# Kernel optimization log

Hardware: AMD Instinct MI355X
Metric: run time of the kernel (lower is better)

## Reference

```python
import jax, jax.numpy as jnp
import numpy as np
import math

B, CIN, COUT, NSC, H, W = 4, 3, 64, 3, 192, 192
HID = 64  # attention hidden channels


def setup_inputs() -> dict:
    key = jax.random.key(0)
    ks = jax.random.split(key, 10)
    pi = math.pi
    return {
        "x": jax.random.normal(ks[0], (B, CIN, H, W), jnp.float32),
        "freq": jax.random.uniform(ks[1], (NSC, COUT, CIN), jnp.float32) * pi,
        "theta": jax.random.uniform(ks[2], (NSC, COUT, CIN), jnp.float32) * pi,
        "sigma": jax.random.uniform(ks[3], (NSC, COUT, CIN), jnp.float32) * pi,
        "f0": jnp.ones((NSC, COUT, CIN), jnp.float32),
        "theta0": jnp.ones((NSC, COUT, CIN), jnp.float32),
        "attn_w1": jax.random.normal(ks[4], (HID, CIN), jnp.float32) / np.sqrt(CIN).astype(np.float32),
        "attn_b1": jnp.zeros((HID,), jnp.float32),
        "attn_w2": jax.random.normal(ks[5], (COUT * NSC, HID), jnp.float32) / np.sqrt(HID).astype(np.float32),
        "attn_b2": jnp.zeros((COUT * NSC,), jnp.float32),
        "bn_w": jnp.ones((COUT * NSC,), jnp.float32),
        "bn_b": jnp.zeros((COUT * NSC,), jnp.float32),
        "mixing_param": jax.random.uniform(ks[6], (1,), jnp.float32),
        "conv_w": jax.random.normal(ks[7], (COUT, CIN, 3, 3), jnp.float32) * 0.1,
        "freq_band_select": jax.random.uniform(ks[8], (COUT, CIN, 2), jnp.float32),
    }


def _forward(x, freq, theta, sigma, f0, theta0, attn_w1, attn_b1, attn_w2,
             attn_b2, bn_w, bn_b, mixing_param, conv_w, freq_band_select):
    b, cin, h, w = x.shape
    # torch.fft.fftshift default dim=None shifts ALL axes (incl. batch/channel)
    Xs = jnp.fft.fftshift(jnp.fft.fft2(x))  # [B,Cin,H,W] complex64

    # ---- multi-scale log-Gabor filter bank g[S,O,I,H,W] ----
    yy, xx = jnp.meshgrid(jnp.linspace(-1.0, 1.0, h), jnp.linspace(-1.0, 1.0, w), indexing="ij")
    r = jnp.sqrt(xx * xx + yy * yy + 1e-6)
    phi = jnp.arctan2(yy, xx)
    f0e = f0[..., None, None]
    sg = sigma[..., None, None]
    th = theta[..., None, None]
    th0 = theta0[..., None, None]
    fr = freq[..., None, None]
    log_gabor = jnp.exp(-(jnp.log(r) - jnp.log(f0e)) ** 2 / (2.0 * jnp.log(sg / f0e) ** 2))
    angular = jnp.exp(-(phi - th) ** 2 / (2.0 * th0 ** 2))
    g = log_gabor * angular * jnp.cos(fr * r) / (2.0 * math.pi * sg ** 2)  # [S,O,I,H,W]

    # ---- frequency attention: 1x1 conv -> ReLU -> 1x1 conv -> BN(train) -> softmax ----
    mag = jnp.abs(Xs)
    h1 = jax.nn.relu(jnp.einsum("oi,bihw->bohw", attn_w1, mag) + attn_b1[None, :, None, None])
    h2 = jnp.einsum("oi,bihw->bohw", attn_w2, h1) + attn_b2[None, :, None, None]
    mu = h2.mean(axis=(0, 2, 3))
    var = h2.var(axis=(0, 2, 3))  # biased, as torch BN training mode
    h2 = (h2 - mu[None, :, None, None]) * jax.lax.rsqrt(var + 1e-5)[None, :, None, None]
    h2 = h2 * bn_w[None, :, None, None] + bn_b[None, :, None, None]
    attn = jax.nn.softmax(h2, axis=1).reshape(b, NSC, COUT, h, w)  # view as [B,S,O,H,W]

    # ---- attention-weighted complex sum over (scale, out, in), then batch ----
    # attended_output(b) = sum_{s,o,i} attn[b,s,o]*g[s,o,i]*Xs[b,i]; torch then
    # sums over Cin and, via the [B,O,B,I,H,W] broadcast + sum(dims 2,3), over batch.
    Wr = jnp.einsum("bsohw,soihw->bihw", attn, g)  # real attention*filter weights
    A_tot = (Wr * Xs).sum(axis=(0, 1))             # [H,W] complex

    # ---- per-(out,in) frequency band mask (same index range on both axes) ----
    idx = jnp.floor((freq_band_select + 1.0) * 0.5 * h).astype(jnp.int32)  # [O,I,2]
    hr = jnp.arange(h)
    c = (hr[None, None, :] >= idx[..., 0:1]) & (hr[None, None, :] < idx[..., 1:2])  # [O,I,H]
    mask = (c[:, :, :, None] & c[:, :, None, :]).astype(jnp.float32)  # [O,I,H,W]
    Msum = mask.sum(axis=1)  # [O,H,W] (sum over Cin)

    # torch builds r[b0,o,b2,i,h,w]=A[b2]*M[o,i], ifftshift(all axes), ifft2,
    # real, sum over (b2,i). Rolls on summed axes commute with the sums, so this
    # equals ifftshift over (b0,o,h,w) of Q[b0,o]=A_tot*Msum[o] (const in b0).
    Q = jnp.broadcast_to((A_tot[None] * Msum.astype(Xs.dtype))[None], (b, COUT, h, w))
    xf = jnp.fft.ifft2(jnp.fft.ifftshift(Q)).real  # [B,O,H,W]

    xs = jax.lax.conv_general_dilated(
        x, conv_w, window_strides=(1, 1), padding=((1, 1), (1, 1)),
        dimension_numbers=("NCHW", "OIHW", "NCHW"))
    return mixing_param * xf + (1.0 - mixing_param) * xs


def reference(x, freq, theta, sigma, f0, theta0, attn_w1, attn_b1, attn_w2,
              attn_b2, bn_w, bn_b, mixing_param, conv_w, freq_band_select):
    return _forward(x, freq, theta, sigma, f0, theta0, attn_w1, attn_b1,
                    attn_w2, attn_b2, bn_w, bn_b, mixing_param, conv_w,
                    freq_band_select)
```

## Files before the change

### kernel.cpp

```cpp
#include <hip/hip_runtime.h>
#include <math.h>

#define NPIX  36864
#define PI2   6.28318530717958647692f

#define TW_OFF    0
#define PCA_OFF   1536
#define PCB_OFF   10752
#define W1F4_OFF  15360
#define W2B_OFF   16384
#define BN_OFF    65536
#define IDX_OFF   67072
#define M2_OFF    68608
#define T1_OFF    85248
#define XS_OFF    3624192
#define AH_OFF    7163136
#define XF_OFF    7458048
#define E2B_OFF   15846656
#define WS_FUSED  7458048
#define WS_SPLIT  16895232

#define PH_BYTES  14155776
#define E2C_OFF   14155776
#define OUT_MIN_ELEMS 9437184

typedef __attribute__((ext_vector_type(8))) short short8;
typedef __attribute__((ext_vector_type(4))) float floatx4;

__device__ __forceinline__ void bf16split(float v, unsigned short& hi, unsigned short& lo) {
    unsigned ub = __builtin_bit_cast(unsigned, v);
    hi = (unsigned short)(ub >> 16);
    float vh = __builtin_bit_cast(float, ub & 0xFFFF0000u);
    lo = (unsigned short)(__builtin_bit_cast(unsigned, v - vh) >> 16);
}

__global__ void k_pre(const float* freq, const float* theta, const float* sigma,
                      const float* f0, const float* theta0, const float* fbs,
                      const float* w1, const float* b1v, const float* w2,
                      char* ws, char* outw, int split) {
    float2* tw   = (float2*)(ws + TW_OFF);
    float4* pcA  = (float4*)(ws + PCA_OFF);
    float2* pcB  = (float2*)(ws + PCB_OFF);
    float4* w1f4 = (float4*)(ws + W1F4_OFF);
    unsigned short* w2b = (unsigned short*)(ws + W2B_OFF);
    int* idx = (int*)(ws + IDX_OFF);
    int gtid = blockIdx.x * blockDim.x + threadIdx.x;
    int gsz  = gridDim.x * blockDim.x;
    for (int n = gtid; n < 192; n += gsz) {
        float th = PI2 * (float)n / 192.0f;
        tw[n] = make_float2(cosf(th), sinf(th));
    }
    for (int t = gtid; t < 576; t += gsz) {
        int s = t / 192, rem = t % 192, o = rem / 3, i = rem % 3;
        float fr = freq[t], th = theta[t], sg = sigma[t], f0v = f0[t], th0 = theta0[t];
        float lg  = logf(sg / f0v);
        float a1  = -1.0f / (2.0f * lg * lg);
        float lf0 = logf(f0v);
        float a2  = -1.0f / (2.0f * th0 * th0);
        float lsc = -logf(PI2 * sg * sg);
        int pidx = (s*3 + i)*64 + o;
        pcA[pidx] = make_float4(a1, lf0, a2, th);
        pcB[pidx] = make_float2(fr, lsc);
    }
    for (int t = gtid; t < 64; t += gsz)
        w1f4[t] = make_float4(w1[t*3+0], w1[t*3+1], w1[t*3+2], b1v[t]);
    for (int u = gtid; u < 24576; u += gsz) {
        int j = u & 7; int v = u >> 3;
        int l = v & 63; v >>= 6;
        int hsel = v & 1; v >>= 1;
        int t = v % 12; int kc = v / 12;
        int k = kc*32 + (l>>4)*8 + j;
        int c = t*16 + (l & 15);
        float wv = w2[c*64 + k];
        unsigned short hi, lo;
        bf16split(wv, hi, lo);
        w2b[u] = hsel ? lo : hi;
    }
    for (int t = gtid; t < 192; t += gsz) {
        int lo = (int)floorf((fbs[t*2+0] + 1.0f) * 0.5f * 192.0f) - 96;
        int hi = (int)floorf((fbs[t*2+1] + 1.0f) * 0.5f * 192.0f) - 96;
        lo = max(0, min(96, lo));
        hi = max(0, min(96, hi));
        if (hi < lo) hi = lo;
        idx[t*2+0] = lo; idx[t*2+1] = hi;
    }
    if (split) {
        unsigned short* e2b = (unsigned short*)(ws + E2B_OFF);
        for (int u = gtid; u < 147456; u += gsz) {
            int j = u & 7;
            int l = (u >> 3) & 63;
            int half = (u >> 9) & 1;
            int rest = u >> 10;
            int kc = rest % 12, t = rest / 12;
            int k = kc*32 + ((l >> 4) << 3) + j;
            int w = k >> 1, comp = k & 1;
            int n = t*16 + (l & 15);
            int ang = (w * n) % 192;
            float th = PI2 * (float)ang / 192.0f;
            float v = comp ? sinf(th) : cosf(th);
            unsigned short hi, lo;
            bf16split(v, hi, lo);
            e2b[u] = half ? lo : hi;
        }
        unsigned short* e2c = (unsigned short*)(outw + E2C_OFF);
        for (int u = gtid; u < 73728; u += gsz) {
            int j = u & 7;
            int l = (u >> 3) & 63;
            int half = (u >> 9) & 1;
            int rest = u >> 10;
            int kc = rest % 6, t = rest / 6;
            int k = kc*32 + ((l >> 4) << 3) + j;
            int w = k >> 1, comp = k & 1;
            int n = t*16 + (l & 15);
            int ang = (w * n) % 192;
            float th = PI2 * (float)ang / 192.0f;
            float v = comp ? sinf(th) : cosf(th);
            unsigned short hi, lo;
            bf16split(v, hi, lo);
            e2c[u] = half ? lo : hi;
        }
    }
}

__global__ __launch_bounds__(192) void k_dft1s(const float* x, char* ws) {
    __shared__ float2 twsh[192];
    const float2* tw = (const float2*)(ws + TW_OFF);
    int tid = threadIdx.x;
    twsh[tid] = tw[tid];
    __syncthreads();
    int bi = blockIdx.x;
    int y0 = blockIdx.y * 4;
    int z  = blockIdx.z;
    float2* t1 = (float2*)(ws + (z ? XF_OFF : T1_OFF));
    int w  = tid;
    const float* xp = x + bi * NPIX;
    float2 acc[4];
#pragma unroll
    for (int d = 0; d < 4; d++) acc[d] = make_float2(0.f, 0.f);
    int h0 = z * 96;
    for (int h = h0; h < h0 + 96; h++) {
        float xv = xp[h*192 + w];
        int m = (h * y0) % 192;
#pragma unroll
        for (int d = 0; d < 4; d++) {
            float2 e = twsh[m];
            acc[d].x += xv * e.x;
            acc[d].y -= xv * e.y;
            m += h; if (m >= 192) m -= 192;
        }
    }
    float2* op = t1 + bi * NPIX;
#pragma unroll
    for (int d = 0; d < 4; d++) op[(y0 + d)*192 + w] = acc[d];
}

__global__ __launch_bounds__(192) void k_dft1(const float* x, char* ws) {
    __shared__ float2 twsh[192];
    const float2* tw = (const float2*)(ws + TW_OFF);
    float2* t1 = (float2*)(ws + T1_OFF);
    int tid = threadIdx.x;
    twsh[tid] = tw[tid];
    __syncthreads();
    int bi = blockIdx.x;
    int y0 = blockIdx.y * 4;
    int w  = tid;
    const float* xp = x + bi * NPIX;
    float2 acc[4];
#pragma unroll
    for (int d = 0; d < 4; d++) acc[d] = make_float2(0.f, 0.f);
    for (int h = 0; h < 192; h++) {
        float xv = xp[h*192 + w];
        int m = (h * y0) % 192;
#pragma unroll
        for (int d = 0; d < 4; d++) {
            float2 e = twsh[m];
            acc[d].x += xv * e.x;
            acc[d].y -= xv * e.y;
            m += h; if (m >= 192) m -= 192;
        }
    }
    float2* op = t1 + bi * NPIX;
#pragma unroll
    for (int d = 0; d < 4; d++) op[(y0 + d)*192 + w] = acc[d];
}

__global__ __launch_bounds__(256) void k_dft2m(char* ws) {
    __shared__ __align__(16) float2 Ar[16][194];
    const float2* t1a = (const float2*)(ws + T1_OFF);
    const float2* t1b = (const float2*)(ws + XF_OFF);
    const unsigned short* e2b = (const unsigned short*)(ws + E2B_OFF);
    float2* Xs = (float2*)(ws + XS_OFF);
    int tid = threadIdx.x;
    int bi = blockIdx.x / 12;
    int y0 = (blockIdx.x % 12) * 16;
    for (int u = tid; u < 3072; u += 256) {
        int m = u / 192, w = u - m*192;
        float2 v = t1a[bi*NPIX + (y0+m)*192 + w];
        float2 v2 = t1b[bi*NPIX + (y0+m)*192 + w];
        v.x += v2.x; v.y += v2.y;
        Ar[m][w] = v;
    }
    __syncthreads();
    int wave = tid >> 6, lane = tid & 63;
    int ml = lane & 15, qd = lane >> 4;
    floatx4 accre[3], accim[3];
#pragma unroll
    for (int tt = 0; tt < 3; tt++) {
        accre[tt] = (floatx4){0.f,0.f,0.f,0.f};
        accim[tt] = (floatx4){0.f,0.f,0.f,0.f};
    }
    union AB { short8 v; unsigned short u[8]; };
#pragma unroll 1
    for (int kc = 0; kc < 12; kc++) {
        int wb = kc*16 + qd*4;
        float4 p01 = *(const float4*)&Ar[ml][wb];
        float4 p23 = *(const float4*)&Ar[ml][wb + 2];
        float av[8]  = {p01.x, p01.y, p01.z, p01.w, p23.x, p23.y, p23.z, p23.w};
        float apv[8] = {p01.y, -p01.x, p01.w, -p01.z, p23.y, -p23.x, p23.w, -p23.z};
        AB ah, al, aph, apl;
#pragma unroll
        for (int j = 0; j < 8; j++) {
            bf16split(av[j],  ah.u[j],  al.u[j]);
            bf16split(apv[j], aph.u[j], apl.u[j]);
        }
#pragma unroll
        for (int tt = 0; tt < 3; tt++) {
            int t = wave*3 + tt;
            const unsigned short* bp = e2b + (((t*12 + kc)*2) << 9) + (lane << 3);
            short8 bh = *(const short8*)bp;
            short8 bl = *(const short8*)(bp + 512);
            floatx4 r = accre[tt];
            r = __builtin_amdgcn_mfma_f32_16x16x32_bf16(ah.v,  bh, r, 0, 0, 0);
            r = __builtin_amdgcn_mfma_f32_16x16x32_bf16(al.v,  bh, r, 0, 0, 0);
            r = __builtin_amdgcn_mfma_f32_16x16x32_bf16(ah.v,  bl, r, 0, 0, 0);
            accre[tt] = r;
            floatx4 q = accim[tt];
            q = __builtin_amdgcn_mfma_f32_16x16x32_bf16(aph.v, bh, q, 0, 0, 0);
            q = __builtin_amdgcn_mfma_f32_16x16x32_bf16(apl.v, bh, q, 0, 0, 0);
            q = __builtin_amdgcn_mfma_f32_16x16x32_bf16(aph.v, bl, q, 0, 0, 0);
            accim[tt] = q;
        }
    }
    int b = bi / 3, i = bi % 3;
    int bs = (b + 2) & 3;
    int is = (i + 1) % 3;
    float2* Xp = Xs + (bs*3 + is)*NPIX;
#pragma unroll
    for (int tt = 0; tt < 3; tt++) {
        int kx = (wave*3 + tt)*16 + ml;
        int ks = kx + 96; if (ks >= 192) ks -= 192;
#pragma unroll
        for (int r = 0; r < 4; r++) {
            int y = y0 + qd*4 + r;
            int ys = y + 96; if (ys >= 192) ys -= 192;
            Xp[ys*192 + ks] = make_float2(accre[tt][r], accim[tt][r]);
        }
    }
}

__global__ __launch_bounds__(192) void k_dft2(char* ws, int split) {
    __shared__ float2 twsh[192];
    __shared__ float2 row[192];
    const float2* tw = (const float2*)(ws + TW_OFF);
    const float2* t1a = (const float2*)(ws + T1_OFF);
    const float2* t1b = (const float2*)(ws + XF_OFF);
    float2* Xs = (float2*)(ws + XS_OFF);
    int tid = threadIdx.x;
    int bi = blockIdx.x, y = blockIdx.y;
    twsh[tid] = tw[tid];
    {
        float2 v = t1a[bi*NPIX + y*192 + tid];
        if (split) {
            float2 v2 = t1b[bi*NPIX + y*192 + tid];
            v.x += v2.x; v.y += v2.y;
        }
        row[tid] = v;
    }
    __syncthreads();
    int kx = tid;
    float2 st = twsh[kx];
    float2 acc = make_float2(0.f, 0.f);
#pragma unroll 1
    for (int w0 = 0; w0 < 192; w0 += 32) {
        float2 e = twsh[(w0 * kx) % 192];
#pragma unroll
        for (int w = 0; w < 32; w++) {
            float2 t = row[w0 + w];
            acc.x += t.x*e.x + t.y*e.y;
            acc.y += t.y*e.x - t.x*e.y;
            float ex = e.x*st.x - e.y*st.y;
            e.y = e.x*st.y + e.y*st.x;
            e.x = ex;
        }
    }
    int b = bi / 3, i = bi % 3;
    int bs = (b + 2) & 3;
    int is = (i + 1) % 3;
    int ys = y + 96;  if (ys >= 192) ys -= 192;
    int ks = kx + 96; if (ks >= 192) ks -= 192;
    Xs[(bs*3 + is)*NPIX + ys*192 + ks] = acc;
}

__global__ __launch_bounds__(256) void k_stats(char* ws) {
    __shared__ float magL[192];
    __shared__ float4 w1L[64];
    __shared__ float m1L[64];
    __shared__ __align__(16) unsigned short fragH[512*8];
    __shared__ __align__(16) unsigned short fragL[512*8];
    const float2* Xs = (const float2*)(ws + XS_OFF);
    float* M2 = (float*)(ws + M2_OFF);
    int tid = threadIdx.x;
    int wave = tid >> 6, lane = tid & 63;
    if (tid < 64) { w1L[tid] = ((const float4*)(ws + W1F4_OFF))[tid]; m1L[tid] = 0.f; }
    __syncthreads();
    int cch = wave*16 + (lane & 15);
    float4 wf = w1L[cch];
    float msum = 0.f;
    floatx4 acc[4];
#pragma unroll
    for (int nb = 0; nb < 4; nb++) acc[nb] = (floatx4){0.f, 0.f, 0.f, 0.f};
    union AB { short8 v; unsigned short u[8]; };
#pragma unroll 1
    for (int it = 0; it < 2; it++) {
        int tile = blockIdx.x * 2 + it;
        int S0 = tile * 64;
        int b = S0 / NPIX;
        int p0 = S0 - b*NPIX;
        if (tid < 192) {
            int i = tid >> 6, s = tid & 63;
            float2 v = Xs[(b*3 + i)*NPIX + p0 + s];
            magL[s*3 + i] = sqrtf(v.x*v.x + v.y*v.y);
        }
        __syncthreads();
#pragma unroll
        for (int kc = 0; kc < 2; kc++) {
            AB h8, l8;
#pragma unroll
            for (int j = 0; j < 8; j++) {
                int s = kc*32 + (lane>>4)*8 + j;
                float mg0 = magL[s*3], mg1 = magL[s*3+1], mg2 = magL[s*3+2];
                float hv = fmaxf(wf.w + wf.x*mg0 + wf.y*mg1 + wf.z*mg2, 0.f);
                msum += hv;
                bf16split(hv, h8.u[j], l8.u[j]);
            }
            int z = (kc*4 + wave)*64 + lane;
            *(short8*)&fragH[z*8] = h8.v;
            *(short8*)&fragL[z*8] = l8.v;
        }
        __syncthreads();
        short8 Ah0 = *(const short8*)&fragH[((0*4+wave)*64 + lane)*8];
        short8 Ah1 = *(const short8*)&fragH[((1*4+wave)*64 + lane)*8];
        short8 Al0 = *(const short8*)&fragL[((0*4+wave)*64 + lane)*8];
        short8 Al1 = *(const short8*)&fragL[((1*4+wave)*64 + lane)*8];
#pragma unroll
        for (int nb = 0; nb < 4; nb++) {
            short8 Bh0 = *(const short8*)&fragH[((0*4+nb)*64 + lane)*8];
            short8 Bh1 = *(const short8*)&fragH[((1*4+nb)*64 + lane)*8];
            short8 Bl0 = *(const short8*)&fragL[((0*4+nb)*64 + lane)*8];
            short8 Bl1 = *(const short8*)&fragL[((1*4+nb)*64 + lane)*8];
            floatx4 a = acc[nb];
            a = __builtin_amdgcn_mfma_f32_16x16x32_bf16(Ah0, Bh0, a, 0, 0, 0);
            a = __builtin_amdgcn_mfma_f32_16x16x32_bf16(Al0, Bh0, a, 0, 0, 0);
            a = __builtin_amdgcn_mfma_f32_16x16x32_bf16(Ah0, Bl0, a, 0, 0, 0);
            a = __builtin_amdgcn_mfma_f32_16x16x32_bf16(Ah1, Bh1, a, 0, 0, 0);
            a = __builtin_amdgcn_mfma_f32_16x16x32_bf16(Al1, Bh1, a, 0, 0, 0);
            a = __builtin_amdgcn_mfma_f32_16x16x32_bf16(Ah1, Bl1, a, 0, 0, 0);
            acc[nb] = a;
        }
        __syncthreads();
    }
#pragma unroll
    for (int nb = 0; nb < 4; nb++)
#pragma unroll
        for (int r = 0; r < 4; r++) {
            int row = wave*16 + (lane>>4)*4 + r;
            int col = nb*16 + (lane & 15);
            atomicAdd(&M2[row*64 + col], acc[nb][r]);
        }
    atomicAdd(&m1L[cch], msum);
    __syncthreads();
    if (tid < 64) atomicAdd(&M2[4096 + tid], m1L[tid]);
}

__global__ __launch_bounds__(64) void k_bn(const float* w2, const float* bnw,
                                           const float* bnb, char* ws) {
    const float* M2 = (const float*)(ws + M2_OFF);
    const float* m1 = M2 + 4096;
    float* bnsc = (float*)(ws + BN_OFF);
    float* bnsh = bnsc + 192;
    int c = blockIdx.x;
    int jj = threadIdx.x;
    const float* row = w2 + c*64;
    float rj = row[jj];
    float inner = 0.f;
    const float* m2r = M2 + jj*64;
    for (int k = 0; k < 64; k++) inner += row[k] * m2r[k];
    float qpart = rj * inner;
    float dpart = rj * m1[jj];
#pragma unroll
    for (int sh = 32; sh >= 1; sh >>= 1) {
        qpart += __shfl_xor(qpart, sh);
        dpart += __shfl_xor(dpart, sh);
    }
    if (jj == 0) {
        const float invN = 1.0f / 147456.0f;
        float d = dpart * invN;
        float qv = qpart * invN;
        float var = qv - d*d;
        float rstd = rsqrtf(var + 1e-5f);
        float scale = bnw[c] * rstd;
        bnsc[c] = scale;
        bnsh[c] = bnb[c] - d * scale;
    }
}

__global__ __launch_bounds__(256) void k_attn(char* ws) {
    __shared__ __align__(16) float4 pcAL[576];
    __shared__ float2 pcBL[576];
    __shared__ float4 w1L[64];
    const float2* Xs = (const float2*)(ws + XS_OFF);
    const float* bnA = (const float*)(ws + BN_OFF);
    const char* W2G = (const char*)(ws + W2B_OFF);
    float2* Ah = (float2*)(ws + AH_OFF);
    int tid = threadIdx.x;
    {
        const float4* pcA4 = (const float4*)(ws + PCA_OFF);
        const float2* pcB2 = (const float2*)(ws + PCB_OFF);
        for (int u = tid; u < 576; u += 256) {
            pcAL[u] = pcA4[u];
            pcBL[u] = pcB2[u];
        }
        if (tid < 64) w1L[tid] = ((const float4*)(ws + W1F4_OFF))[tid];
    }
    __syncthreads();
    int wave = tid >> 6, lane = tid & 63;
    int cl = lane & 15, q = lane >> 4;
    int g = blockIdx.x * 4 + wave;
    int pix0 = g * 4;

    union AB { short8 v; unsigned short u[8]; };
    int pb = pix0 + (cl >> 2), bb = cl & 3;
    float2 q0 = Xs[(bb*3+0)*NPIX + pb];
    float2 q1 = Xs[(bb*3+1)*NPIX + pb];
    float2 q2 = Xs[(bb*3+2)*NPIX + pb];
    float mg0 = sqrtf(q0.x*q0.x + q0.y*q0.y);
    float mg1 = sqrtf(q1.x*q1.x + q1.y*q1.y);
    float mg2 = sqrtf(q2.x*q2.x + q2.y*q2.y);
    AB ah[2], al[2];
#pragma unroll
    for (int kc = 0; kc < 2; kc++)
#pragma unroll
        for (int j = 0; j < 8; j++) {
            int k = kc*32 + q*8 + j;
            float4 wf = w1L[k];
            float hv = fmaxf(wf.w + wf.x*mg0 + wf.y*mg1 + wf.z*mg2, 0.f);
            bf16split(hv, ah[kc].u[j], al[kc].u[j]);
        }
    int pixE = pix0 + q;
    int hh = pixE / 192, ww = pixE - hh*192;
    float yy = -1.0f + (float)hh * (2.0f/191.0f);
    float xx = -1.0f + (float)ww * (2.0f/191.0f);
    float rr = sqrtf(xx*xx + yy*yy + 1e-6f);
    float lr = __logf(rr);
    float phi = atan2f(yy, xx);
    float sm0 = 0.f, sm1 = 0.f, sm2 = 0.f, sm3 = 0.f;
    float Wr[4][3];
#pragma unroll
    for (int r = 0; r < 4; r++) { Wr[r][0] = 0.f; Wr[r][1] = 0.f; Wr[r][2] = 0.f; }
#pragma unroll 2
    for (int t = 0; t < 12; t++) {
        floatx4 a = {0.f, 0.f, 0.f, 0.f};
#pragma unroll
        for (int kc = 0; kc < 2; kc++) {
            int ob = (((kc*12 + t)*2)*64 + lane)*16;
            short8 bh = *(const short8*)(W2G + ob);
            short8 bl = *(const short8*)(W2G + ob + 1024);
            a = __builtin_amdgcn_mfma_f32_16x16x32_bf16(ah[kc].v, bh, a, 0, 0, 0);
            a = __builtin_amdgcn_mfma_f32_16x16x32_bf16(al[kc].v, bh, a, 0, 0, 0);
            a = __builtin_amdgcn_mfma_f32_16x16x32_bf16(ah[kc].v, bl, a, 0, 0, 0);
        }
        int c = t*16 + cl;
        float sc_ = bnA[c], sh_ = bnA[192 + c];
        float e0 = __expf(a[0]*sc_ + sh_);
        float e1 = __expf(a[1]*sc_ + sh_);
        float e2 = __expf(a[2]*sc_ + sh_);
        float e3 = __expf(a[3]*sc_ + sh_);
        sm0 += e0; sm1 += e1; sm2 += e2; sm3 += e3;
        int sB = c >> 6, o = c & 63;
#pragma unroll
        for (int i = 0; i < 3; i++) {
            int pidx = (sB*3 + i)*64 + o;
            float4 pa = pcAL[pidx];
            float2 pbv = pcBL[pidx];
            float dl = lr - pa.y, dp = phi - pa.w;
            float gv = __expf(pa.x*dl*dl + pa.z*dp*dp + pbv.y) * __cosf(pbv.x*rr);
            Wr[0][i] += e0*gv; Wr[1][i] += e1*gv;
            Wr[2][i] += e2*gv; Wr[3][i] += e3*gv;
        }
    }
#pragma unroll
    for (int sh = 1; sh < 16; sh <<= 1) {
        sm0 += __shfl_xor(sm0, sh); sm1 += __shfl_xor(sm1, sh);
        sm2 += __shfl_xor(sm2, sh); sm3 += __shfl_xor(sm3, sh);
    }
    float inv0 = 1.0f/sm0, inv1 = 1.0f/sm1, inv2 = 1.0f/sm2, inv3 = 1.0f/sm3;
    float are = 0.f, aim = 0.f;
#pragma unroll
    for (int i = 0; i < 3; i++) {
        float2 x0 = Xs[(0*3+i)*NPIX + pixE];
        float2 x1 = Xs[(1*3+i)*NPIX + pixE];
        float2 x2 = Xs[(2*3+i)*NPIX + pixE];
        float2 x3 = Xs[(3*3+i)*NPIX + pixE];
        float w0v = Wr[0][i]*inv0, w1v = Wr[1][i]*inv1;
        float w2v = Wr[2][i]*inv2, w3v = Wr[3][i]*inv3;
        are += w0v*x0.x + w1v*x1.x + w2v*x2.x + w3v*x3.x;
        aim += w0v*x0.y + w1v*x1.y + w2v*x2.y + w3v*x3.y;
    }
#pragma unroll
    for (int sh = 1; sh < 16; sh <<= 1) {
        are += __shfl_xor(are, sh);
        aim += __shfl_xor(aim, sh);
    }
    if (cl == 0) {
        int hs = hh + 96; if (hs >= 192) hs -= 192;
        int wsx = ww + 96; if (wsx >= 192) wsx -= 192;
        Ah[hs*192 + wsx] = make_float2(are, aim);
    }
}

__global__ __launch_bounds__(192) void k_phpre(char* ws, char* outw) {
    __shared__ float2 AhL[96];
    const float2* tw  = (const float2*)(ws + TW_OFF);
    const float2* Ahp = (const float2*)(ws + AH_OFF);
    float2* Ph = (float2*)outw;
    int y = threadIdx.x;
    int w = blockIdx.x;
    if (y < 96) AhL[y] = Ahp[y*192 + w];
    __syncthreads();
    float2 step = tw[y];
    float ex = 1.f, ey = 0.f;
    float ax = 0.f, ay = 0.f;
    for (int h = 0; h < 96; h++) {
        float2 a = AhL[h];
        ax += a.x*ex - a.y*ey;
        ay += a.x*ey + a.y*ex;
        Ph[(h*96 + w)*192 + y] = make_float2(ax, ay);
        float t = ex*step.x - ey*step.y;
        ey = ex*step.y + ey*step.x;
        ex = t;
    }
}

__global__ __launch_bounds__(256) void k_ifftm(char* ws, char* outw) {
    __shared__ __align__(16) unsigned short AhiL[16*200];
    __shared__ __align__(16) unsigned short AloL[16*200];
    __shared__ int iL[3], iH[3];
    const float2* Ph = (const float2*)outw;
    const unsigned short* e2c = (const unsigned short*)(outw + E2C_OFF);
    const int* idx = (const int*)(ws + IDX_OFF);
    float* xf = (float*)(ws + XF_OFF);
    int tid = threadIdx.x;
    int o  = blockIdx.x / 12;
    int ys = blockIdx.x % 12;
    int op = (o + 32) & 63;
    if (tid < 3) { iL[tid] = idx[(op*3 + tid)*2]; iH[tid] = idx[(op*3 + tid)*2 + 1]; }
    __syncthreads();
    for (int u = tid; u < 1536; u += 256) {
        int w = u >> 4, yy = u & 15;
        int y = ys*16 + yy;
        float sr = 0.f, si = 0.f;
#pragma unroll
        for (int i = 0; i < 3; i++) {
            int lo = iL[i], hi = iH[i];
            if (w >= lo && w < hi) {
                float2 a = Ph[((hi-1)*96 + w)*192 + y];
                sr += a.x; si += a.y;
                if (lo > 0) {
                    float2 b2 = Ph[((lo-1)*96 + w)*192 + y];
                    sr -= b2.x; si -= b2.y;
                }
            }
        }
        unsigned short rh, rl, ih, il;
        bf16split(sr, rh, rl);
        bf16split(-si, ih, il);
        *(unsigned*)&AhiL[yy*200 + 2*w] = (unsigned)rh | ((unsigned)ih << 16);
        *(unsigned*)&AloL[yy*200 + 2*w] = (unsigned)rl | ((unsigned)il << 16);
    }
    __syncthreads();
    int wave = tid >> 6, lane = tid & 63;
    int ml = lane & 15, qd = lane >> 4;
    const float s = 1.0f / 36864.0f;
#pragma unroll 1
    for (int ntl = 0; ntl < 3; ntl++) {
        int nt = wave*3 + ntl;
        floatx4 acc = (floatx4){0.f,0.f,0.f,0.f};
#pragma unroll
        for (int kc = 0; kc < 6; kc++) {
            const unsigned short* bp = e2c + ((nt*6 + kc) << 10) + (lane << 3);
            short8 bh = *(const short8*)bp;
            short8 bl = *(const short8*)(bp + 512);
            int ka = kc*32 + qd*8;
            short8 ah = *(const short8*)&AhiL[ml*200 + ka];
            short8 al = *(const short8*)&AloL[ml*200 + ka];
            acc = __builtin_amdgcn_mfma_f32_16x16x32_bf16(ah, bh, acc, 0, 0, 0);
            acc = __builtin_amdgcn_mfma_f32_16x16x32_bf16(al, bh, acc, 0, 0, 0);
            acc = __builtin_amdgcn_mfma_f32_16x16x32_bf16(ah, bl, acc, 0, 0, 0);
        }
#pragma unroll
        for (int r = 0; r < 4; r++) {
            int y = ys*16 + qd*4 + r;
            int x = nt*16 + ml;
            xf[o*NPIX + y*192 + x] = acc[r] * s;
        }
    }
}

__global__ __launch_bounds__(192) void k_conv(const float* x, const float* convw,
                                              const float* mixp, const float* xf,
                                              float* out) {
    int col = threadIdx.x;
    int y = blockIdx.x;
    int b = blockIdx.y;
    float xv[27];
#pragma unroll
    for (int i = 0; i < 3; i++)
#pragma unroll
        for (int dy = 0; dy < 3; dy++)
#pragma unroll
            for (int dx = 0; dx < 3; dx++) {
                int yq = y + dy - 1, xq = col + dx - 1;
                bool ok = (yq >= 0) & (yq < 192) & (xq >= 0) & (xq < 192);
                xv[(i*3 + dy)*3 + dx] = ok ? x[(b*3+i)*NPIX + yq*192 + xq] : 0.f;
            }
    float mixv = mixp[0];
    float onem = 1.0f - mixv;
    for (int o = 0; o < 64; o++) {
        float s = 0.f;
#pragma unroll
        for (int c = 0; c < 27; c++) s += xv[c] * convw[o*27 + c];
        float xfv = xf[o*NPIX + y*192 + col];
        out[((b*64 + o)*192 + y)*192 + col] = mixv*xfv + onem*s;
    }
}

__global__ __launch_bounds__(192) void k_final(const float* x, const float* convw,
                                               const float* mixp, float* out, char* ws) {
    __shared__ float2 twsh[192];
    __shared__ float2 Ssh[3][96];
    __shared__ float cwsh[27];
    __shared__ int iL[3], iH[3];
    const float2* tw = (const float2*)(ws + TW_OFF);
    const int* idx = (const int*)(ws + IDX_OFF);
    const float2* Ah = (const float2*)(ws + AH_OFF);
    int tid = threadIdx.x;
    int y = blockIdx.x;
    int o = blockIdx.y;
    int op = (o + 32) & 63;
    twsh[tid] = tw[tid];
    if (tid < 27) cwsh[tid] = convw[o*27 + tid];
    if (tid < 3) { iL[tid] = idx[(op*3 + tid)*2]; iH[tid] = idx[(op*3 + tid)*2 + 1]; }
    __syncthreads();
    int l0 = iL[0], u0 = iH[0], l1 = iL[1], u1 = iH[1], l2 = iL[2], u2 = iH[2];
    int n0 = u0 - l0, n1 = u1 - l1, n2 = u2 - l2;
    int p1 = n0 + n1, T = p1 + n2;
    for (int t = tid; t < T; t += 192) {
        int i, off, lo, hi;
        if (t < n0)      { i = 0; off = t;      lo = l0; hi = u0; }
        else if (t < p1) { i = 1; off = t - n0; lo = l1; hi = u1; }
        else             { i = 2; off = t - p1; lo = l2; hi = u2; }
        int wq = lo + off;
        float sx = 0.f, sy = 0.f;
        int m = (lo * y) % 192;
        for (int hq = lo; hq < hi; hq++) {
            float2 a = Ah[hq*192 + wq];
            float2 e = twsh[m];
            sx += a.x*e.x - a.y*e.y;
            sy += a.x*e.y + a.y*e.x;
            m += y; if (m >= 192) m -= 192;
        }
        Ssh[i][off] = make_float2(sx, sy);
    }
    __syncthreads();
    int col = tid;
    float accre = 0.f;
#pragma unroll
    for (int i = 0; i < 3; i++) {
        int lo = iL[i];
        int wi = iH[i] - lo;
        int m = (lo * col) % 192;
        for (int off = 0; off < wi; off++) {
            float2 S = Ssh[i][off];
            float2 e = twsh[m];
            accre += S.x*e.x - S.y*e.y;
            m += col; if (m >= 192) m -= 192;
        }
    }
    float xfv = accre * (1.0f / 36864.0f);
    float mixv = mixp[0];
    float onem = 1.0f - mixv;
#pragma unroll
    for (int b = 0; b < 4; b++) {
        float s = 0.f;
#pragma unroll
        for (int i = 0; i < 3; i++) {
            const float* xp = x + (b*3 + i)*NPIX;
#pragma unroll
            for (int dy = -1; dy <= 1; dy++) {
                int yq = y + dy;
                if (yq < 0 || yq >= 192) continue;
                const float* rowp = xp + yq*192;
#pragma unroll
                for (int dx = -1; dx <= 1; dx++) {
                    int xq = col + dx;
                    if (xq < 0 || xq >= 192) continue;
                    s += rowp[xq] * cwsh[i*9 + (dy+1)*3 + (dx+1)];
                }
            }
        }
        out[((b*64 + o)*192 + y)*192 + col] = mixv*xfv + onem*s;
    }
}

extern "C" void kernel_launch(void* const* d_in, const int* in_sizes, int n_in,
                              void* d_out, int out_size, void* d_ws, size_t ws_size,
                              hipStream_t stream) {
    const float* x      = (const float*)d_in[0];
    const float* freq   = (const float*)d_in[1];
    const float* theta  = (const float*)d_in[2];
    const float* sigma  = (const float*)d_in[3];
    const float* f0     = (const float*)d_in[4];
    const float* theta0 = (const float*)d_in[5];
    const float* aw1    = (const float*)d_in[6];
    const float* ab1    = (const float*)d_in[7];
    const float* aw2    = (const float*)d_in[8];
    const float* bnw    = (const float*)d_in[10];
    const float* bnb    = (const float*)d_in[11];
    const float* mixp   = (const float*)d_in[12];
    const float* convw  = (const float*)d_in[13];
    const float* fbs    = (const float*)d_in[14];
    float* out = (float*)d_out;
    char* ws = (char*)d_ws;
    char* outc = (char*)d_out;
    if (ws_size < (size_t)WS_FUSED) return;
    int split = (ws_size >= (size_t)WS_SPLIT) && (out_size >= OUT_MIN_ELEMS);

    hipMemsetAsync(ws + M2_OFF, 0, 16640, stream);
    k_pre  <<<80, 256, 0, stream>>>(freq, theta, sigma, f0, theta0, fbs,
                                    aw1, ab1, aw2, ws, outc, split);
    if (split) {
        k_dft1s<<<dim3(12, 48, 2), 192, 0, stream>>>(x, ws);
        k_dft2m<<<144, 256, 0, stream>>>(ws);
    } else {
        k_dft1 <<<dim3(12, 48), 192, 0, stream>>>(x, ws);
        k_dft2 <<<dim3(12, 192), 192, 0, stream>>>(ws, 0);
    }
    k_stats<<<1152, 256, 0, stream>>>(ws);
    k_bn   <<<192, 64, 0, stream>>>(aw2, bnw, bnb, ws);
    k_attn <<<2304, 256, 0, stream>>>(ws);
    if (split) {
        k_phpre<<<96, 192, 0, stream>>>(ws, outc);
        k_ifftm<<<768, 256, 0, stream>>>(ws, outc);
        k_conv <<<dim3(192, 4), 192, 0, stream>>>(x, convw, mixp,
                                                  (const float*)(ws + XF_OFF), out);
    } else {
        k_final<<<dim3(192, 64), 192, 0, stream>>>(x, convw, mixp, out, ws);
    }
}
```

Measured before the change: 271.7 us.

## Fuse row DFT into column MFMA kernel using bf16-split twiddle matrices

```diff
diff --git a/kernel.cpp b/kernel.cpp
--- a/kernel.cpp
+++ b/kernel.cpp
@@ -102,6 +102,24 @@
             bf16split(v, hi, lo);
             e2b[u] = half ? lo : hi;
         }
+        unsigned short* e1 = (unsigned short*)(ws + T1_OFF);
+        for (int u = gtid; u < 147456; u += gsz) {
+            int j = u & 7;
+            int l = (u >> 3) & 63;
+            int half = (u >> 9) & 1;
+            int rest = u >> 10;
+            int kc = rest % 6;
+            int comp = (rest / 6) & 1;
+            int yt = rest / 12;
+            int y = yt*16 + (l & 15);
+            int h = kc*32 + ((l >> 4) << 3) + j;
+            int ang = (h * y) % 192;
+            float th = PI2 * (float)ang / 192.0f;
+            float v = comp ? -sinf(th) : cosf(th);
+            unsigned short hi, lo;
+            bf16split(v, hi, lo);
+            e1[u] = half ? lo : hi;
+        }
         unsigned short* e2c = (unsigned short*)(outw + E2C_OFF);
         for (int u = gtid; u < 73728; u += gsz) {
             int j = u & 7;
@@ -122,94 +140,69 @@
     }
 }
 
-__global__ __launch_bounds__(192) void k_dft1s(const float* x, char* ws) {
-    __shared__ float2 twsh[192];
-    const float2* tw = (const float2*)(ws + TW_OFF);
-    int tid = threadIdx.x;
-    twsh[tid] = tw[tid];
-    __syncthreads();
-    int bi = blockIdx.x;
-    int y0 = blockIdx.y * 4;
-    int z  = blockIdx.z;
-    float2* t1 = (float2*)(ws + (z ? XF_OFF : T1_OFF));
-    int w  = tid;
-    const float* xp = x + bi * NPIX;
-    float2 acc[4];
-#pragma unroll
-    for (int d = 0; d < 4; d++) acc[d] = make_float2(0.f, 0.f);
-    int h0 = z * 96;
-    for (int h = h0; h < h0 + 96; h++) {
-        float xv = xp[h*192 + w];
-        int m = (h * y0) % 192;
-#pragma unroll
-        for (int d = 0; d < 4; d++) {
-            float2 e = twsh[m];
-            acc[d].x += xv * e.x;
-            acc[d].y -= xv * e.y;
-            m += h; if (m >= 192) m -= 192;
-        }
-    }
-    float2* op = t1 + bi * NPIX;
-#pragma unroll
-    for (int d = 0; d < 4; d++) op[(y0 + d)*192 + w] = acc[d];
-}
-
-__global__ __launch_bounds__(192) void k_dft1(const float* x, char* ws) {
-    __shared__ float2 twsh[192];
-    const float2* tw = (const float2*)(ws + TW_OFF);
-    float2* t1 = (float2*)(ws + T1_OFF);
-    int tid = threadIdx.x;
-    twsh[tid] = tw[tid];
-    __syncthreads();
-    int bi = blockIdx.x;
-    int y0 = blockIdx.y * 4;
-    int w  = tid;
-    const float* xp = x + bi * NPIX;
-    float2 acc[4];
-#pragma unroll
-    for (int d = 0; d < 4; d++) acc[d] = make_float2(0.f, 0.f);
-    for (int h = 0; h < 192; h++) {
-        float xv = xp[h*192 + w];
-        int m = (h * y0) % 192;
-#pragma unroll
-        for (int d = 0; d < 4; d++) {
-            float2 e = twsh[m];
-            acc[d].x += xv * e.x;
-            acc[d].y -= xv * e.y;
-            m += h; if (m >= 192) m -= 192;
-        }
-    }
-    float2* op = t1 + bi * NPIX;
-#pragma unroll
-    for (int d = 0; d < 4; d++) op[(y0 + d)*192 + w] = acc[d];
-}
-
-__global__ __launch_bounds__(256) void k_dft2m(char* ws) {
+__global__ __launch_bounds__(256) void k_dftm(const float* x, char* ws) {
     __shared__ __align__(16) float2 Ar[16][194];
-    const float2* t1a = (const float2*)(ws + T1_OFF);
-    const float2* t1b = (const float2*)(ws + XF_OFF);
+    const unsigned short* e1  = (const unsigned short*)(ws + T1_OFF);
     const unsigned short* e2b = (const unsigned short*)(ws + E2B_OFF);
     float2* Xs = (float2*)(ws + XS_OFF);
     int tid = threadIdx.x;
     int bi = blockIdx.x / 12;
-    int y0 = (blockIdx.x % 12) * 16;
-    for (int u = tid; u < 3072; u += 256) {
-        int m = u / 192, w = u - m*192;
-        float2 v = t1a[bi*NPIX + (y0+m)*192 + w];
-        float2 v2 = t1b[bi*NPIX + (y0+m)*192 + w];
-        v.x += v2.x; v.y += v2.y;
-        Ar[m][w] = v;
-    }
-    __syncthreads();
+    int yt = blockIdx.x % 12;
+    int y0 = yt * 16;
     int wave = tid >> 6, lane = tid & 63;
     int ml = lane & 15, qd = lane >> 4;
+    const float* xp = x + bi * NPIX;
+    union AB { short8 v; unsigned short u[8]; };
+    floatx4 s1re[3], s1im[3];
+#pragma unroll
+    for (int tt = 0; tt < 3; tt++) {
+        s1re[tt] = (floatx4){0.f,0.f,0.f,0.f};
+        s1im[tt] = (floatx4){0.f,0.f,0.f,0.f};
+    }
+#pragma unroll 1
+    for (int kc = 0; kc < 6; kc++) {
+        const unsigned short* ac = e1 + (((((yt*2 + 0)*6 + kc)*2) << 9) + (lane << 3));
+        const unsigned short* as = e1 + (((((yt*2 + 1)*6 + kc)*2) << 9) + (lane << 3));
+        short8 ach = *(const short8*)ac;
+        short8 acl = *(const short8*)(ac + 512);
+        short8 ash = *(const short8*)as;
+        short8 asl = *(const short8*)(as + 512);
+#pragma unroll
+        for (int tt = 0; tt < 3; tt++) {
+            int nt = wave*3 + tt;
+            AB bh8, bl8;
+#pragma unroll
+            for (int j = 0; j < 8; j++) {
+                int h = kc*32 + qd*8 + j;
+                float xv = xp[h*192 + nt*16 + ml];
+                bf16split(xv, bh8.u[j], bl8.u[j]);
+            }
+            floatx4 r = s1re[tt];
+            r = __builtin_amdgcn_mfma_f32_16x16x32_bf16(ach, bh8.v, r, 0, 0, 0);
+            r = __builtin_amdgcn_mfma_f32_16x16x32_bf16(acl, bh8.v, r, 0, 0, 0);
+            r = __builtin_amdgcn_mfma_f32_16x16x32_bf16(ach, bl8.v, r, 0, 0, 0);
+            s1re[tt] = r;
+            floatx4 q = s1im[tt];
+            q = __builtin_amdgcn_mfma_f32_16x16x32_bf16(ash, bh8.v, q, 0, 0, 0);
+            q = __builtin_amdgcn_mfma_f32_16x16x32_bf16(asl, bh8.v, q, 0, 0, 0);
+            q = __builtin_amdgcn_mfma_f32_16x16x32_bf16(ash, bl8.v, q, 0, 0, 0);
+            s1im[tt] = q;
+        }
+    }
+#pragma unroll
+    for (int tt = 0; tt < 3; tt++) {
+        int w = (wave*3 + tt)*16 + ml;
+#pragma unroll
+        for (int r = 0; r < 4; r++)
+            Ar[qd*4 + r][w] = make_float2(s1re[tt][r], s1im[tt][r]);
+    }
+    __syncthreads();
     floatx4 accre[3], accim[3];
 #pragma unroll
     for (int tt = 0; tt < 3; tt++) {
         accre[tt] = (floatx4){0.f,0.f,0.f,0.f};
         accim[tt] = (floatx4){0.f,0.f,0.f,0.f};
     }
-    union AB { short8 v; unsigned short u[8]; };
 #pragma unroll 1
     for (int kc = 0; kc < 12; kc++) {
         int wb = kc*16 + qd*4;
@@ -258,24 +251,46 @@
     }
 }
 
-__global__ __launch_bounds__(192) void k_dft2(char* ws, int split) {
+__global__ __launch_bounds__(192) void k_dft1(const float* x, char* ws) {
+    __shared__ float2 twsh[192];
+    const float2* tw = (const float2*)(ws + TW_OFF);
+    float2* t1 = (float2*)(ws + T1_OFF);
+    int tid = threadIdx.x;
+    twsh[tid] = tw[tid];
+    __syncthreads();
+    int bi = blockIdx.x;
+    int y0 = blockIdx.y * 4;
+    int w  = tid;
+    const float* xp = x + bi * NPIX;
+    float2 acc[4];
+#pragma unroll
+    for (int d = 0; d < 4; d++) acc[d] = make_float2(0.f, 0.f);
+    for (int h = 0; h < 192; h++) {
+        float xv = xp[h*192 + w];
+        int m = (h * y0) % 192;
+#pragma unroll
+        for (int d = 0; d < 4; d++) {
+            float2 e = twsh[m];
+            acc[d].x += xv * e.x;
+            acc[d].y -= xv * e.y;
+            m += h; if (m >= 192) m -= 192;
+        }
+    }
+    float2* op = t1 + bi * NPIX;
+#pragma unroll
+    for (int d = 0; d < 4; d++) op[(y0 + d)*192 + w] = acc[d];
+}
+
+__global__ __launch_bounds__(192) void k_dft2(char* ws) {
     __shared__ float2 twsh[192];
     __shared__ float2 row[192];
     const float2* tw = (const float2*)(ws + TW_OFF);
     const float2* t1a = (const float2*)(ws + T1_OFF);
-    const float2* t1b = (const float2*)(ws + XF_OFF);
     float2* Xs = (float2*)(ws + XS_OFF);
     int tid = threadIdx.x;
     int bi = blockIdx.x, y = blockIdx.y;
     twsh[tid] = tw[tid];
-    {
-        float2 v = t1a[bi*NPIX + y*192 + tid];
-        if (split) {
-            float2 v2 = t1b[bi*NPIX + y*192 + tid];
-            v.x += v2.x; v.y += v2.y;
-        }
-        row[tid] = v;
-    }
+    row[tid] = t1a[bi*NPIX + y*192 + tid];
     __syncthreads();
     int kx = tid;
     float2 st = twsh[kx];
@@ -746,14 +761,13 @@
     int split = (ws_size >= (size_t)WS_SPLIT) && (out_size >= OUT_MIN_ELEMS);
 
     hipMemsetAsync(ws + M2_OFF, 0, 16640, stream);
-    k_pre  <<<80, 256, 0, stream>>>(freq, theta, sigma, f0, theta0, fbs,
-                                    aw1, ab1, aw2, ws, outc, split);
+    k_pre  <<<192, 256, 0, stream>>>(freq, theta, sigma, f0, theta0, fbs,
+                                     aw1, ab1, aw2, ws, outc, split);
     if (split) {
-        k_dft1s<<<dim3(12, 48, 2), 192, 0, stream>>>(x, ws);
-        k_dft2m<<<144, 256, 0, stream>>>(ws);
+        k_dftm <<<144, 256, 0, stream>>>(x, ws);
     } else {
         k_dft1 <<<dim3(12, 48), 192, 0, stream>>>(x, ws);
-        k_dft2 <<<dim3(12, 192), 192, 0, stream>>>(ws, 0);
+        k_dft2 <<<dim3(12, 192), 192, 0, stream>>>(ws);
     }
     k_stats<<<1152, 256, 0, stream>>>(ws);
     k_bn   <<<192, 64, 0, stream>>>(aw2, bnw, bnb, ws);
```

New measurement: 244.3 us. -10.1%, faster.
